# Performance work log

Hardware: AMD Instinct MI355X
Metric: run time of the kernel (lower is better)

## Reference

```python
import jax, jax.numpy as jnp
import numpy as np


def setup_inputs() -> dict:
    key = jax.random.key(0)
    k1, k2 = jax.random.split(key)
    B, C, H, W = 32, 256, 32, 32
    K = 2048
    x = jax.random.normal(k1, (B, C, H, W), dtype=jnp.float32)
    # nn.Embedding init in source is uniform(-1/K, 1/K); use normal scaled similarly-small
    embed_w = jax.random.uniform(k2, (K, C), dtype=jnp.float32, minval=-1.0 / K, maxval=1.0 / K)
    return {"x": x, "embed_w": embed_w}


def reference(x, embed_w):
    # x: [B, C, H, W] -> tokens [B, HW, C]
    B, C, H, W = x.shape
    tokens = jnp.transpose(x, (0, 2, 3, 1)).reshape(B, H * W, C)
    # Euclidean argmin: argmin_k ||t - e_k||^2 = argmin_k (||e_k||^2 - 2 t.e_k)
    # Avoids materializing sqrt cdist; argmin is identical.
    e_sq = jnp.sum(embed_w * embed_w, axis=-1)           # [K]
    dots = jnp.einsum('bnc,kc->bnk', tokens, embed_w)    # [B, HW, K] dominant intermediate
    embed_idx = jnp.argmin(e_sq[None, None, :] - 2.0 * dots, axis=-1)  # [B, HW]
    # one-hot matmul in source == gather
    quantized = embed_w[embed_idx]                        # [B, HW, C]
    quantize = jnp.transpose(quantized.reshape(B, H, W, C), (0, 3, 1, 2))  # [B, C, H, W]
    embed_index = embed_idx.reshape(B, H, W)
    loss = jnp.zeros((1,), dtype=jnp.float32)  # eval path: loss stays 0
    return quantize, embed_index, loss
```

## Files before the change

kernel.cpp:

```cpp
#include <hip/hip_runtime.h>


#define CDIM 256
#define KDIM 2048
#define HW   1024
#define NTOK 32768
#define QOFF 8388608
#define LOFF (QOFF + NTOK)

typedef _Float16 f16x8 __attribute__((ext_vector_type(8)));
typedef float    f32x4 __attribute__((ext_vector_type(4)));

__device__ __forceinline__ f16x8 ld16(const char* p) { return *(const f16x8*)(p); }

__global__ __launch_bounds__(256) void prep_kernel(const float* __restrict__ x,
                                                   const float* __restrict__ ew,
                                                   char* __restrict__ Aws,
                                                   char* __restrict__ Ews,
                                                   float* __restrict__ esq,
                                                   float* __restrict__ out) {
    __shared__ float tile[32][257];
    const int t = threadIdx.x;
    if (blockIdx.x < 1024) {
        const int bid = blockIdx.x;
        const int b = bid >> 5;
        const int kc = (bid >> 2) & 7;
        const int c0 = kc * 32;
        const int hw0 = (bid & 3) * 256;
        #pragma unroll 8
        for (int r = 0; r < 32; ++r)
            tile[r][t] = x[((size_t)(b * CDIM + c0 + r) << 10) + hw0 + t];
        __syncthreads();
        union { _Float16 h[32]; uint4 q[4]; } Hb, Lb;
        #pragma unroll 8
        for (int r = 0; r < 32; ++r) {
            const float xs = tile[r][t] * 64.0f;
            const _Float16 hh = (_Float16)xs;
            Hb.h[r] = hh;
            Lb.h[r] = (_Float16)(xs - (float)hh);
        }
        const int tok = b * HW + hw0 + t;
        const int p = tok >> 6, row = tok & 63;
        char* d = Aws + (size_t)p * 65536 + kc * 8192 + row * 16;
        #pragma unroll
        for (int g = 0; g < 4; ++g) {
            *(uint4*)(d + g * 1024)        = Hb.q[g];
            *(uint4*)(d + 4096 + g * 1024) = Lb.q[g];
        }
    } else {
        const int bid = blockIdx.x - 1024;
        const int code = bid * 8 + (t >> 5);
        const int u = t & 31;
        const float4 v0 = *(const float4*)&ew[(size_t)code * CDIM + u * 8];
        const float4 v1 = *(const float4*)&ew[(size_t)code * CDIM + u * 8 + 4];
        float s = v0.x*v0.x + v0.y*v0.y + v0.z*v0.z + v0.w*v0.w
                + v1.x*v1.x + v1.y*v1.y + v1.z*v1.z + v1.w*v1.w;
        #pragma unroll
        for (int m = 16; m >= 1; m >>= 1) s += __shfl_xor(s, m, 32);
        if (u == 0) esq[code] = s * 2097152.0f;
        const float e[8] = {v0.x, v0.y, v0.z, v0.w, v1.x, v1.y, v1.z, v1.w};
        union { _Float16 h[8]; uint4 q; } H, L;
        #pragma unroll
        for (int j = 0; j < 8; ++j) {
            const float ev = e[j] * 32768.0f;
            const _Float16 hh = (_Float16)ev;
            H.h[j] = hh;
            L.h[j] = (_Float16)(ev - (float)hh);
        }
        const int kc = u >> 2, g = u & 3;
        const int p = code >> 6, row = code & 63;
        char* d = Ews + (size_t)p * 65536 + kc * 8192 + g * 1024 + row * 16;
        *(uint4*)d = H.q;
        *(uint4*)(d + 4096) = L.q;
        if (bid == 0 && t == 0) out[LOFF] = 0.0f;
    }
}

__global__ __launch_bounds__(256, 4) void vqmm_kernel(const char* __restrict__ Aws,
                                                      const char* __restrict__ Ews,
                                                      const float* __restrict__ esq,
                                                      float* __restrict__ cv,
                                                      int* __restrict__ ci) {
    __shared__ __align__(16) char elds[32768];

    const int t = threadIdx.x;
    const int bid = blockIdx.x;
    const int by = (bid & 7) | ((bid >> 8) << 3);
    const int bx = (bid >> 3) & 31;
    const int lane = t & 63, w = t >> 6;
    const int g = lane >> 4, lr = lane & 15;
    const int kc0 = (bid + w) & 3;

    const char* pa = Aws + (size_t)(by * 2 + (w >> 1)) * 65536
                   + g * 1024 + ((w & 1) * 32 + lr) * 16;
    const char* esrc = Ews + (size_t)bx * 65536;

    f16x8 fa[2], fb[2], ec[4], ed[4];
    {
        const char* pa0 = pa + kc0 * 8192;
        #pragma unroll
        for (int m = 0; m < 2; ++m) {
            fa[m] = ld16(pa0 + m * 256);
            fb[m] = ld16(pa0 + 4096 + m * 256);
        }
    }
    #pragma unroll
    for (int j = 0; j < 8; ++j) {
        const int off = j * 4096 + t * 16;
        *(uint4*)(elds + off) = *(const uint4*)(esrc + off);
    }
    __syncthreads();

    const f32x4 zf = {0.f, 0.f, 0.f, 0.f};
    f32x4 acc[2][4];
    #pragma unroll
    for (int m = 0; m < 2; ++m)
        #pragma unroll
        for (int n = 0; n < 4; ++n) acc[m][n] = zf;

    const char* el0 = elds + g * 1024 + lr * 16;
    {
        const char* ep0 = el0 + kc0 * 8192;
        #pragma unroll
        for (int n = 0; n < 4; ++n) {
            ec[n] = ld16(ep0 + n * 256);
            ed[n] = ld16(ep0 + 4096 + n * 256);
        }
    }

    #pragma unroll
    for (int h = 0; h < 2; ++h) {
        if (h == 1) {
            __syncthreads();
            #pragma unroll
            for (int j = 0; j < 8; ++j) {
                const int off = j * 4096 + t * 16;
                *(uint4*)(elds + off) = *(const uint4*)(esrc + 32768 + off);
            }
            __syncthreads();
            const char* ep = el0 + kc0 * 8192;
            #pragma unroll
            for (int n = 0; n < 4; ++n) {
                ec[n] = ld16(ep + n * 256);
                ed[n] = ld16(ep + 4096 + n * 256);
            }
        }
        #pragma unroll
        for (int i = 0; i < 4; ++i) {
            const bool lastA = (h == 1) && (i == 3);
            const int gkcn = (i < 3) ? (h * 4 + ((kc0 + i + 1) & 3)) : (4 + kc0);
            const char* pan = pa + gkcn * 8192;
            #pragma unroll
            for (int m = 0; m < 2; ++m) {
                __builtin_amdgcn_s_setprio(1);
                #pragma unroll
                for (int n = 0; n < 4; ++n) {
                    acc[m][n] = __builtin_amdgcn_mfma_f32_16x16x32_f16(fa[m], ec[n], acc[m][n], 0, 0, 0);
                    acc[m][n] = __builtin_amdgcn_mfma_f32_16x16x32_f16(fa[m], ed[n], acc[m][n], 0, 0, 0);
                    acc[m][n] = __builtin_amdgcn_mfma_f32_16x16x32_f16(fb[m], ec[n], acc[m][n], 0, 0, 0);
                }
                __builtin_amdgcn_s_setprio(0);
                if (!lastA) {
                    fa[m] = ld16(pan + m * 256);
                    fb[m] = ld16(pan + 4096 + m * 256);
                }
            }
            if (i < 3) {
                const char* en = el0 + ((kc0 + i + 1) & 3) * 8192;
                #pragma unroll
                for (int n = 0; n < 4; ++n) {
                    ec[n] = ld16(en + n * 256);
                    ed[n] = ld16(en + 4096 + n * 256);
                }
            }
        }
    }

    float eq[4];
    #pragma unroll
    for (int n = 0; n < 4; ++n) eq[n] = esq[bx * 64 + n * 16 + lr];
    #pragma unroll
    for (int m = 0; m < 2; ++m) {
        #pragma unroll
        for (int r = 0; r < 4; ++r) {
            float bv = 3.4e38f; int bi = 0x7fffffff;
            #pragma unroll
            for (int n = 0; n < 4; ++n) {
                const float d = fmaf(-2.0f, acc[m][n][r], eq[n]);
                const int cidx = bx * 64 + n * 16 + lr;
                if (d < bv) { bv = d; bi = cidx; }
            }
            #pragma unroll
            for (int mk = 1; mk < 16; mk <<= 1) {
                const float ov = __shfl_xor(bv, mk, 16);
                const int   oi = __shfl_xor(bi, mk, 16);
                if (ov < bv || (ov == bv && oi < bi)) { bv = ov; bi = oi; }
            }
            if (lr == 0) {
                const size_t o = (size_t)bx * NTOK + by * 128 + w * 32 + m * 16 + g * 4 + r;
                cv[o] = bv; ci[o] = bi;
            }
        }
    }
}

__global__ __launch_bounds__(256) void merge_gather_kernel(const float* __restrict__ cv,
                                                           const int* __restrict__ ci,
                                                           const float* __restrict__ ew,
                                                           float* __restrict__ out) {
    __shared__ int sIdx[64];
    const int t = threadIdx.x;
    const int n0 = blockIdx.x * 64;
    if (t < 64) {
        const int tok = n0 + t;
        float bv = cv[tok]; int bi = ci[tok];
        #pragma unroll
        for (int s = 1; s < 32; ++s) {
            const float v = cv[(size_t)s * NTOK + tok];
            const int   i2 = ci[(size_t)s * NTOK + tok];
            if (v < bv || (v == bv && i2 < bi)) { bv = v; bi = i2; }
        }
        sIdx[t] = bi;
        out[QOFF + tok] = (float)bi;
    }
    __syncthreads();
    const int b = n0 >> 10, hw0 = n0 & (HW - 1);
    const int i = t & 63, cg = t >> 6;
    const int kidx = sIdx[i];
    const float* er = ew + (size_t)kidx * CDIM;
    float* ob = out + (size_t)b * CDIM * HW + hw0 + i;
    #pragma unroll
    for (int p = 0; p < CDIM / 4; ++p) {
        const int c = cg * 64 + p;
        ob[(size_t)c * HW] = er[c];
    }
}

extern "C" void kernel_launch(void* const* d_in, const int* in_sizes, int n_in,
                              void* d_out, int out_size, void* d_ws, size_t ws_size,
                              hipStream_t stream) {
    const float* x  = (const float*)d_in[0];
    const float* ew = (const float*)d_in[1];
    float* out = (float*)d_out;
    char* ws = (char*)d_ws;

    char*  Aws = ws;
    char*  Ews = ws + 33554432;
    float* esq = (float*)(ws + 35651584);
    float* cvv = (float*)(ws + 35659776);
    int*   cii = (int*)(ws + 39854080);

    prep_kernel<<<1280, 256, 0, stream>>>(x, ew, Aws, Ews, esq, out);
    vqmm_kernel<<<8192, 256, 0, stream>>>(Aws, Ews, esq, cvv, cii);
    merge_gather_kernel<<<NTOK / 64, 256, 0, stream>>>(cvv, cii, ew, out);
}
```

Before: 151.6 us.

## Switch VQ distance GEMM to 32x32x16 MFMA with larger per-block token tile

Replaces the 16x16x32 f16 MFMA tiles with 32x32x16 MFMAs, so each wave computes a 64-token by 64-code tile and each block covers 256 tokens. The workspace layouts for tokens and codebook are reorganized to match the 32-row operand pattern. The grid is halved and launch bounds drop to 3 waves-per-SIMD occupancy. E operand reloads are split between the two accumulator groups. The intent is to reduce operand loads and instruction count per FLOP and to reuse shared-memory codebook tiles across more tokens. In exchange, register pressure is higher and occupancy is lower.

Result: slower. 210.3 us (+38.7%).

```diff
diff --git a/kernel.cpp b/kernel.cpp
--- a/kernel.cpp
+++ b/kernel.cpp
@@ -8,8 +8,8 @@
 #define QOFF 8388608
 #define LOFF (QOFF + NTOK)
 
-typedef _Float16 f16x8 __attribute__((ext_vector_type(8)));
-typedef float    f32x4 __attribute__((ext_vector_type(4)));
+typedef _Float16 f16x8  __attribute__((ext_vector_type(8)));
+typedef float    f32x16 __attribute__((ext_vector_type(16)));
 
 __device__ __forceinline__ f16x8 ld16(const char* p) { return *(const f16x8*)(p); }
 
@@ -40,12 +40,12 @@
             Lb.h[r] = (_Float16)(xs - (float)hh);
         }
         const int tok = b * HW + hw0 + t;
-        const int p = tok >> 6, row = tok & 63;
-        char* d = Aws + (size_t)p * 65536 + kc * 8192 + row * 16;
+        const int p = tok >> 6, rowtile = (tok >> 5) & 1, row = tok & 31;
+        char* d = Aws + (size_t)p * 65536 + kc * 8192 + rowtile * 2048 + row * 16;
         #pragma unroll
         for (int g = 0; g < 4; ++g) {
-            *(uint4*)(d + g * 1024)        = Hb.q[g];
-            *(uint4*)(d + 4096 + g * 1024) = Lb.q[g];
+            *(uint4*)(d + g * 512)        = Hb.q[g];
+            *(uint4*)(d + 4096 + g * 512) = Lb.q[g];
         }
     } else {
         const int bid = blockIdx.x - 1024;
@@ -67,16 +67,16 @@
             H.h[j] = hh;
             L.h[j] = (_Float16)(ev - (float)hh);
         }
-        const int kc = u >> 2, g = u & 3;
-        const int p = code >> 6, row = code & 63;
-        char* d = Ews + (size_t)p * 65536 + kc * 8192 + g * 1024 + row * 16;
+        const int kc = u >> 2, sub = u & 3;
+        const int p = code >> 6, ntile = (code >> 5) & 1, crow = code & 31;
+        char* d = Ews + (size_t)p * 65536 + kc * 8192 + ntile * 2048 + sub * 512 + crow * 16;
         *(uint4*)d = H.q;
         *(uint4*)(d + 4096) = L.q;
         if (bid == 0 && t == 0) out[LOFF] = 0.0f;
     }
 }
 
-__global__ __launch_bounds__(256, 4) void vqmm_kernel(const char* __restrict__ Aws,
+__global__ __launch_bounds__(256, 3) void vqmm_kernel(const char* __restrict__ Aws,
                                                       const char* __restrict__ Ews,
                                                       const float* __restrict__ esq,
                                                       float* __restrict__ cv,
@@ -88,21 +88,24 @@
     const int by = (bid & 7) | ((bid >> 8) << 3);
     const int bx = (bid >> 3) & 31;
     const int lane = t & 63, w = t >> 6;
-    const int g = lane >> 4, lr = lane & 15;
+    const int l5 = lane >> 5, l31 = lane & 31;
     const int kc0 = (bid + w) & 3;
 
-    const char* pa = Aws + (size_t)(by * 2 + (w >> 1)) * 65536
-                   + g * 1024 + ((w & 1) * 32 + lr) * 16;
+    const int lanebase = l5 * 512 + l31 * 16;
+    const char* pa = Aws + (size_t)(by * 4 + w) * 65536 + lanebase;
     const char* esrc = Ews + (size_t)bx * 65536;
-
-    f16x8 fa[2], fb[2], ec[4], ed[4];
+    const char* el0 = elds + lanebase;
+
+    f16x8 fa[2][2], fb[2][2], ec[2][2], ed[2][2];
     {
         const char* pa0 = pa + kc0 * 8192;
         #pragma unroll
-        for (int m = 0; m < 2; ++m) {
-            fa[m] = ld16(pa0 + m * 256);
-            fb[m] = ld16(pa0 + 4096 + m * 256);
-        }
+        for (int m = 0; m < 2; ++m)
+            #pragma unroll
+            for (int s = 0; s < 2; ++s) {
+                fa[m][s] = ld16(pa0 + m * 2048 + s * 1024);
+                fb[m][s] = ld16(pa0 + 4096 + m * 2048 + s * 1024);
+            }
     }
     #pragma unroll
     for (int j = 0; j < 8; ++j) {
@@ -111,22 +114,26 @@
     }
     __syncthreads();
 
-    const f32x4 zf = {0.f, 0.f, 0.f, 0.f};
-    f32x4 acc[2][4];
+    f32x16 acc[2][2];
     #pragma unroll
     for (int m = 0; m < 2; ++m)
         #pragma unroll
-        for (int n = 0; n < 4; ++n) acc[m][n] = zf;
-
-    const char* el0 = elds + g * 1024 + lr * 16;
+        for (int n = 0; n < 2; ++n)
+            #pragma unroll
+            for (int r = 0; r < 16; ++r) acc[m][n][r] = 0.0f;
+
     {
         const char* ep0 = el0 + kc0 * 8192;
         #pragma unroll
-        for (int n = 0; n < 4; ++n) {
-            ec[n] = ld16(ep0 + n * 256);
-            ed[n] = ld16(ep0 + 4096 + n * 256);
-        }
-    }
+        for (int n = 0; n < 2; ++n)
+            #pragma unroll
+            for (int s = 0; s < 2; ++s) {
+                ec[n][s] = ld16(ep0 + n * 2048 + s * 1024);
+                ed[n][s] = ld16(ep0 + 4096 + n * 2048 + s * 1024);
+            }
+    }
+
+#define MFMA32(A, B, C) C = __builtin_amdgcn_mfma_f32_32x32x16_f16(A, B, C, 0, 0, 0)
 
     #pragma unroll
     for (int h = 0; h < 2; ++h) {
@@ -140,64 +147,93 @@
             __syncthreads();
             const char* ep = el0 + kc0 * 8192;
             #pragma unroll
-            for (int n = 0; n < 4; ++n) {
-                ec[n] = ld16(ep + n * 256);
-                ed[n] = ld16(ep + 4096 + n * 256);
-            }
+            for (int n = 0; n < 2; ++n)
+                #pragma unroll
+                for (int s = 0; s < 2; ++s) {
+                    ec[n][s] = ld16(ep + n * 2048 + s * 1024);
+                    ed[n][s] = ld16(ep + 4096 + n * 2048 + s * 1024);
+                }
         }
         #pragma unroll
         for (int i = 0; i < 4; ++i) {
-            const bool lastA = (h == 1) && (i == 3);
-            const int gkcn = (i < 3) ? (h * 4 + ((kc0 + i + 1) & 3)) : (4 + kc0);
+            const bool last_i = (i == 3);
+            const bool reloadA = !(h == 1 && last_i);
+            const bool reloadE = !last_i;
+            const int kcl_n = (kc0 + i + 1) & 3;
+            const int gkcn = last_i ? (4 + kc0) : (h * 4 + kcl_n);
             const char* pan = pa + gkcn * 8192;
+            const char* en = el0 + kcl_n * 8192;
+
+            __builtin_amdgcn_s_setprio(1);
             #pragma unroll
             for (int m = 0; m < 2; ++m) {
-                __builtin_amdgcn_s_setprio(1);
-                #pragma unroll
-                for (int n = 0; n < 4; ++n) {
-                    acc[m][n] = __builtin_amdgcn_mfma_f32_16x16x32_f16(fa[m], ec[n], acc[m][n], 0, 0, 0);
-                    acc[m][n] = __builtin_amdgcn_mfma_f32_16x16x32_f16(fa[m], ed[n], acc[m][n], 0, 0, 0);
-                    acc[m][n] = __builtin_amdgcn_mfma_f32_16x16x32_f16(fb[m], ec[n], acc[m][n], 0, 0, 0);
+                MFMA32(fa[m][0], ec[0][0], acc[m][0]);
+                MFMA32(fa[m][1], ec[0][1], acc[m][0]);
+                MFMA32(fa[m][0], ed[0][0], acc[m][0]);
+                MFMA32(fa[m][1], ed[0][1], acc[m][0]);
+                MFMA32(fb[m][0], ec[0][0], acc[m][0]);
+                MFMA32(fb[m][1], ec[0][1], acc[m][0]);
+            }
+            __builtin_amdgcn_s_setprio(0);
+            if (reloadE) {
+                #pragma unroll
+                for (int s = 0; s < 2; ++s) {
+                    ec[0][s] = ld16(en + s * 1024);
+                    ed[0][s] = ld16(en + 4096 + s * 1024);
                 }
-                __builtin_amdgcn_s_setprio(0);
-                if (!lastA) {
-                    fa[m] = ld16(pan + m * 256);
-                    fb[m] = ld16(pan + 4096 + m * 256);
+            }
+            __builtin_amdgcn_s_setprio(1);
+            #pragma unroll
+            for (int m = 0; m < 2; ++m) {
+                MFMA32(fa[m][0], ec[1][0], acc[m][1]);
+                MFMA32(fa[m][1], ec[1][1], acc[m][1]);
+                MFMA32(fa[m][0], ed[1][0], acc[m][1]);
+                MFMA32(fa[m][1], ed[1][1], acc[m][1]);
+                MFMA32(fb[m][0], ec[1][0], acc[m][1]);
+                MFMA32(fb[m][1], ec[1][1], acc[m][1]);
+            }
+            __builtin_amdgcn_s_setprio(0);
+            if (reloadA) {
+                #pragma unroll
+                for (int m = 0; m < 2; ++m)
+                    #pragma unroll
+                    for (int s = 0; s < 2; ++s) {
+                        fa[m][s] = ld16(pan + m * 2048 + s * 1024);
+                        fb[m][s] = ld16(pan + 4096 + m * 2048 + s * 1024);
+                    }
+            }
+            if (reloadE) {
+                #pragma unroll
+                for (int s = 0; s < 2; ++s) {
+                    ec[1][s] = ld16(en + 2048 + s * 1024);
+                    ed[1][s] = ld16(en + 4096 + 2048 + s * 1024);
                 }
             }
-            if (i < 3) {
-                const char* en = el0 + ((kc0 + i + 1) & 3) * 8192;
-                #pragma unroll
-                for (int n = 0; n < 4; ++n) {
-                    ec[n] = ld16(en + n * 256);
-                    ed[n] = ld16(en + 4096 + n * 256);
-                }
-            }
-        }
-    }
-
-    float eq[4];
-    #pragma unroll
-    for (int n = 0; n < 4; ++n) eq[n] = esq[bx * 64 + n * 16 + lr];
+        }
+    }
+#undef MFMA32
+
+    float eq[2];
+    eq[0] = esq[bx * 64 + l31];
+    eq[1] = esq[bx * 64 + 32 + l31];
     #pragma unroll
     for (int m = 0; m < 2; ++m) {
         #pragma unroll
-        for (int r = 0; r < 4; ++r) {
-            float bv = 3.4e38f; int bi = 0x7fffffff;
-            #pragma unroll
-            for (int n = 0; n < 4; ++n) {
-                const float d = fmaf(-2.0f, acc[m][n][r], eq[n]);
-                const int cidx = bx * 64 + n * 16 + lr;
-                if (d < bv) { bv = d; bi = cidx; }
-            }
-            #pragma unroll
-            for (int mk = 1; mk < 16; mk <<= 1) {
-                const float ov = __shfl_xor(bv, mk, 16);
-                const int   oi = __shfl_xor(bi, mk, 16);
+        for (int r = 0; r < 16; ++r) {
+            const float d0 = fmaf(-2.0f, acc[m][0][r], eq[0]);
+            const float d1 = fmaf(-2.0f, acc[m][1][r], eq[1]);
+            float bv; int bi;
+            if (d1 < d0) { bv = d1; bi = bx * 64 + 32 + l31; }
+            else         { bv = d0; bi = bx * 64 + l31; }
+            #pragma unroll
+            for (int mk = 1; mk < 32; mk <<= 1) {
+                const float ov = __shfl_xor(bv, mk);
+                const int   oi = __shfl_xor(bi, mk);
                 if (ov < bv || (ov == bv && oi < bi)) { bv = ov; bi = oi; }
             }
-            if (lr == 0) {
-                const size_t o = (size_t)bx * NTOK + by * 128 + w * 32 + m * 16 + g * 4 + r;
+            if (l31 == 0) {
+                const size_t o = (size_t)bx * NTOK + by * 256 + w * 64
+                               + m * 32 + (r & 3) + 8 * (r >> 2) + 4 * l5;
                 cv[o] = bv; ci[o] = bi;
             }
         }
@@ -251,6 +287,6 @@
     int*   cii = (int*)(ws + 39854080);
 
     prep_kernel<<<1280, 256, 0, stream>>>(x, ew, Aws, Ews, esq, out);
-    vqmm_kernel<<<8192, 256, 0, stream>>>(Aws, Ews, esq, cvv, cii);
+    vqmm_kernel<<<4096, 256, 0, stream>>>(Aws, Ews, esq, cvv, cii);
     merge_gather_kernel<<<NTOK / 64, 256, 0, stream>>>(cvv, cii, ew, out);
 }
```
